# Kernel tuning notes

Hardware: AMD Instinct MI355X
Metric: run time of the kernel (lower is better)

Reference implementation:

```python
import jax, jax.numpy as jnp
import numpy as np

B, N_ATOMS = 8192, 64      # molecules, atoms per molecule
DIM, EXTRA, N_CLS = 70, 7, 11
N_FP = 10000               # fingerprint vocab


def setup_inputs() -> dict:
    key = jax.random.key(0)
    ks = jax.random.split(key, 9)
    atoms = jax.random.randint(ks[0], (B, N_ATOMS), 0, N_FP, dtype=jnp.int64 if jax.config.jax_enable_x64 else jnp.int32)
    adjacency = jax.random.uniform(ks[1], (B, N_ATOMS, N_ATOMS), dtype=jnp.float32)
    sel_desc = jax.random.normal(ks[2], (B, EXTRA), dtype=jnp.float32)
    embed_table = jax.random.normal(ks[3], (N_FP, DIM), dtype=jnp.float32)
    w1 = jax.random.normal(ks[4], (DIM, DIM), dtype=jnp.float32) * 0.05
    b1 = jax.random.normal(ks[5], (DIM,), dtype=jnp.float32) * 0.05
    w2 = jax.random.normal(ks[6], (DIM, DIM), dtype=jnp.float32) * 0.05
    b2 = jax.random.normal(ks[7], (DIM,), dtype=jnp.float32) * 0.05
    wp = jax.random.normal(ks[8], (DIM + EXTRA, N_CLS), dtype=jnp.float32) * 0.05
    bp = jnp.zeros((N_CLS,), dtype=jnp.float32)
    return {"atoms": atoms, "adjacency": adjacency, "sel_desc": sel_desc,
            "embed_table": embed_table, "w1": w1, "b1": b1,
            "w2": w2, "b2": b2, "wp": wp, "bp": bp}


def reference(atoms, adjacency, sel_desc, embed_table, w1, b1, w2, b2, wp, bp):
    # embed atoms: [B, n, dim]
    x = embed_table[atoms]
    # message-passing layers: relu(linear) then (block-diagonal == batched) adjacency matmul
    for w, b in ((w1, b1), (w2, b2)):
        h = jax.nn.relu(jnp.einsum('bnd,de->bne', x, w) + b)
        x = jnp.einsum('bnm,bmd->bnd', adjacency, h)
    # segment-sum pool over atoms per molecule (sum_axis)
    y = jnp.sum(x, axis=1)                       # [B, dim]
    y = jnp.concatenate([y, sel_desc], axis=1)   # [B, dim+extra]
    return jnp.einsum('bd,dc->bc', y, wp) + bp   # [B, 11]
```

## Files before the change

kernel.cpp:

```cpp
#include <hip/hip_runtime.h>
#include <hip/hip_bf16.h>

#define NFP    10000
#define DIM    70
#define GPAD   72
#define NATOMS 64
#define PGROWS 16

typedef short  short8  __attribute__((ext_vector_type(8)));
typedef float  floatx4 __attribute__((ext_vector_type(4)));

__device__ inline unsigned short f2bf(float f) {
  union { float f; unsigned u; } x; x.f = f;
  unsigned r = x.u + 0x7fffu + ((x.u >> 16) & 1u);
  return (unsigned short)(r >> 16);
}

__device__ inline ushort2 pk2bf(float a, float b) {
  __hip_bfloat162 h = __float22bfloat162_rn(make_float2(a, b));
  union { __hip_bfloat162 h; ushort2 u; } c; c.h = h; return c.u;
}

__global__ __launch_bounds__(256) void precompute_G(
    const float* __restrict__ emb, const float* __restrict__ w1,
    const float* __restrict__ b1,  const float* __restrict__ w2,
    unsigned short* __restrict__ G) {
  __shared__ float w1s[DIM * GPAD];
  __shared__ float w2s[DIM * GPAD];
  __shared__ float b1s[GPAD];
  __shared__ float embs[PGROWS * GPAD];
  __shared__ float e1s[PGROWS * GPAD];
  const int t = threadIdx.x;

  for (int i = t; i < DIM * GPAD; i += 256) {
    int r = i / GPAD, c = i % GPAD;
    float v1 = 0.f, v2 = 0.f;
    if (c < DIM) { v1 = w1[r * DIM + c]; v2 = w2[r * DIM + c]; }
    w1s[i] = v1; w2s[i] = v2;
  }
  if (t < GPAD) b1s[t] = (t < DIM) ? b1[t] : 0.f;
  const int row0 = blockIdx.x * PGROWS;
  for (int i = t; i < PGROWS * GPAD; i += 256) {
    int r = i / GPAD, c = i % GPAD;
    int vr = row0 + r;
    embs[i] = (vr < NFP && c < DIM) ? emb[vr * DIM + c] : 0.f;
  }
  __syncthreads();

  for (int task = t; task < PGROWS * 18; task += 256) {
    int r = task / 18, c4 = (task % 18) * 4;
    float4 acc = *(const float4*)&b1s[c4];
    for (int k = 0; k < DIM; k++) {
      float e = embs[r * GPAD + k];
      float4 w = *(const float4*)&w1s[k * GPAD + c4];
      acc.x = fmaf(e, w.x, acc.x); acc.y = fmaf(e, w.y, acc.y);
      acc.z = fmaf(e, w.z, acc.z); acc.w = fmaf(e, w.w, acc.w);
    }
    acc.x = fmaxf(acc.x, 0.f); acc.y = fmaxf(acc.y, 0.f);
    acc.z = fmaxf(acc.z, 0.f); acc.w = fmaxf(acc.w, 0.f);
    *(float4*)&e1s[r * GPAD + c4] = acc;
  }
  __syncthreads();

  for (int task = t; task < PGROWS * 18; task += 256) {
    int r = task / 18, c4 = (task % 18) * 4;
    int vr = row0 + r;
    if (vr >= NFP) continue;
    float ax = 0.f, ay = 0.f, az = 0.f, aw = 0.f;
    for (int k = 0; k < DIM; k++) {
      float e = e1s[r * GPAD + k];
      float4 w = *(const float4*)&w2s[k * GPAD + c4];
      ax = fmaf(e, w.x, ax); ay = fmaf(e, w.y, ay);
      az = fmaf(e, w.z, az); aw = fmaf(e, w.w, aw);
    }
    unsigned short* gp = G + vr * GPAD + c4;
    gp[0] = f2bf(ax); gp[1] = f2bf(ay); gp[2] = f2bf(az); gp[3] = f2bf(aw);
  }
}

__global__ __launch_bounds__(256, 6) void mol_fused(
    const int* __restrict__ atoms, const float* __restrict__ adj,
    const float* __restrict__ sel, const float* __restrict__ b2,
    const float* __restrict__ wp,  const float* __restrict__ bp,
    const unsigned short* __restrict__ G, float* __restrict__ out) {
  __shared__ unsigned short adjs[64 * GPAD];
  __shared__ unsigned short gTs[80 * GPAD];
  __shared__ float cwave[4 * 64];
  __shared__ float yacc[4 * 80];

  const int b = blockIdx.x;
  const int t = threadIdx.x;
  const int w = t >> 6, lane = t & 63;
  const int q = lane >> 4, li = lane & 15;
  const int R = w * 16;
  const int m = lane;

  const float* ap = adj + (size_t)b * 4096;
  const int mc = (t & 15) * 4;
  const int a  = t >> 4;
  float4 v0 = *(const float4*)(ap + (a     ) * 64 + mc);
  float4 v1 = *(const float4*)(ap + (a + 16) * 64 + mc);
  float4 v2 = *(const float4*)(ap + (a + 32) * 64 + mc);
  float4 v3 = *(const float4*)(ap + (a + 48) * 64 + mc);
  const int myAtom = atoms[b * 64 + m];
  const uint4* Gv = (const uint4*)G;
  uint4 g0 = Gv[(unsigned)myAtom * 9 + w];
  uint4 g1 = Gv[(unsigned)myAtom * 9 + w + 4];
  uint4 g2; g2.x = g2.y = g2.z = g2.w = 0u;
  if (w == 0) g2 = Gv[(unsigned)myAtom * 9 + 8];

  {
    float4 cs;
    cs.x = (v0.x + v1.x) + (v2.x + v3.x);
    cs.y = (v0.y + v1.y) + (v2.y + v3.y);
    cs.z = (v0.z + v1.z) + (v2.z + v3.z);
    cs.w = (v0.w + v1.w) + (v2.w + v3.w);
#pragma unroll
    for (int s = 16; s <= 32; s <<= 1) {
      cs.x += __shfl_xor(cs.x, s); cs.y += __shfl_xor(cs.y, s);
      cs.z += __shfl_xor(cs.z, s); cs.w += __shfl_xor(cs.w, s);
    }
    if (((t >> 4) & 3) == 0) *(float4*)&cwave[w * 64 + mc] = cs;

    float4 vv[4] = {v0, v1, v2, v3};
#pragma unroll
    for (int it = 0; it < 4; it++) {
      int n = a + 16 * it;
      ushort2 lo = pk2bf(vv[it].x, vv[it].y);
      ushort2 hi = pk2bf(vv[it].z, vv[it].w);
      ushort4 u; u.x = lo.x; u.y = lo.y; u.z = hi.x; u.w = hi.y;
      *(ushort4*)&adjs[n * GPAD + mc] = u;
    }
  }

  {
    unsigned short* gp0 = &gTs[(w * 8) * GPAD + m];
    gp0[0 * GPAD] = (unsigned short)(g0.x & 0xffff);
    gp0[1 * GPAD] = (unsigned short)(g0.x >> 16);
    gp0[2 * GPAD] = (unsigned short)(g0.y & 0xffff);
    gp0[3 * GPAD] = (unsigned short)(g0.y >> 16);
    gp0[4 * GPAD] = (unsigned short)(g0.z & 0xffff);
    gp0[5 * GPAD] = (unsigned short)(g0.z >> 16);
    gp0[6 * GPAD] = (unsigned short)(g0.w & 0xffff);
    gp0[7 * GPAD] = (unsigned short)(g0.w >> 16);
    unsigned short* gp1 = &gTs[((w + 4) * 8) * GPAD + m];
    gp1[0 * GPAD] = (unsigned short)(g1.x & 0xffff);
    gp1[1 * GPAD] = (unsigned short)(g1.x >> 16);
    gp1[2 * GPAD] = (unsigned short)(g1.y & 0xffff);
    gp1[3 * GPAD] = (unsigned short)(g1.y >> 16);
    gp1[4 * GPAD] = (unsigned short)(g1.z & 0xffff);
    gp1[5 * GPAD] = (unsigned short)(g1.z >> 16);
    gp1[6 * GPAD] = (unsigned short)(g1.w & 0xffff);
    gp1[7 * GPAD] = (unsigned short)(g1.w >> 16);
    if (w == 0) {
      unsigned short* gp2 = &gTs[64 * GPAD + m];
      gp2[0 * GPAD] = (unsigned short)(g2.x & 0xffff);
      gp2[1 * GPAD] = (unsigned short)(g2.x >> 16);
      gp2[2 * GPAD] = (unsigned short)(g2.y & 0xffff);
      gp2[3 * GPAD] = (unsigned short)(g2.y >> 16);
      gp2[4 * GPAD] = (unsigned short)(g2.z & 0xffff);
      gp2[5 * GPAD] = (unsigned short)(g2.z >> 16);
      gp2[6 * GPAD] = (unsigned short)(g2.w & 0xffff);
      gp2[7 * GPAD] = (unsigned short)(g2.w >> 16);
    }
  }
  __syncthreads();

  float cr[4];
  {
    float4 c0 = *(const float4*)&cwave[      R + q * 4];
    float4 c1 = *(const float4*)&cwave[ 64 + R + q * 4];
    float4 c2 = *(const float4*)&cwave[128 + R + q * 4];
    float4 c3 = *(const float4*)&cwave[192 + R + q * 4];
    cr[0] = (c0.x + c1.x) + (c2.x + c3.x);
    cr[1] = (c0.y + c1.y) + (c2.y + c3.y);
    cr[2] = (c0.z + c1.z) + (c2.z + c3.z);
    cr[3] = (c0.w + c1.w) + (c2.w + c3.w);
  }
  float bbv[5];
#pragma unroll
  for (int nt = 0; nt < 5; nt++) {
    int d = nt * 16 + li;
    bbv[nt] = (d < DIM) ? b2[d] : 0.f;
  }

  short8 a0 = *(const short8*)&adjs[(R + li) * GPAD + q * 8];
  short8 a1 = *(const short8*)&adjs[(R + li) * GPAD + 32 + q * 8];
  floatx4 acc[5];
#pragma unroll
  for (int nt = 0; nt < 5; nt++) {
    floatx4 z = {0.f, 0.f, 0.f, 0.f};
    short8 b0 = *(const short8*)&gTs[(nt * 16 + li) * GPAD + q * 8];
    short8 b1 = *(const short8*)&gTs[(nt * 16 + li) * GPAD + 32 + q * 8];
    z = __builtin_amdgcn_mfma_f32_16x16x32_bf16(a0, b0, z, 0, 0, 0);
    z = __builtin_amdgcn_mfma_f32_16x16x32_bf16(a1, b1, z, 0, 0, 0);
    acc[nt] = z;
  }

#pragma unroll
  for (int nt = 0; nt < 5; nt++) {
    float bb = bbv[nt];
    float p = 0.f;
#pragma unroll
    for (int r = 0; r < 4; r++)
      p = fmaf(cr[r], fmaxf(acc[nt][r] + bb, 0.f), p);
    p += __shfl_xor(p, 16);
    p += __shfl_xor(p, 32);
    if (q == 0) yacc[w * 80 + nt * 16 + li] = p;
  }
  __syncthreads();

  if (w == 0) {
    float* yv = cwave;
    yv[lane] = yacc[lane] + yacc[80 + lane] + yacc[160 + lane] + yacc[240 + lane];
    if (lane < 16) {
      int d2 = 64 + lane;
      float v2s = 0.f;
      if (lane < 6)
        v2s = yacc[d2] + yacc[80 + d2] + yacc[160 + d2] + yacc[240 + d2];
      else if (lane < 13)
        v2s = sel[(size_t)b * 7 + (d2 - DIM)];
      yv[d2] = v2s;
    }
    int c = lane & 15, qq = lane >> 4;
    float accp = 0.f;
    if (c < 11) {
#pragma unroll
      for (int j = 0; j < 20; j++) {
        int d = qq + 4 * j;
        int dd = (d < 77) ? d : 76;
        accp = fmaf(yv[d], wp[dd * 11 + c], accp);
      }
    }
    accp += __shfl_xor(accp, 16);
    accp += __shfl_xor(accp, 32);
    if (lane < 11) out[(size_t)b * 11 + lane] = accp + bp[lane];
  }
}

extern "C" void kernel_launch(void* const* d_in, const int* in_sizes, int n_in,
                              void* d_out, int out_size, void* d_ws, size_t ws_size,
                              hipStream_t stream) {
  const int*   atoms = (const int*)d_in[0];
  const float* adj   = (const float*)d_in[1];
  const float* sel   = (const float*)d_in[2];
  const float* emb   = (const float*)d_in[3];
  const float* w1    = (const float*)d_in[4];
  const float* b1    = (const float*)d_in[5];
  const float* w2    = (const float*)d_in[6];
  const float* b2    = (const float*)d_in[7];
  const float* wp    = (const float*)d_in[8];
  const float* bp    = (const float*)d_in[9];

  const int B = in_sizes[0] / NATOMS;
  unsigned short* G = (unsigned short*)d_ws;

  precompute_G<<<(NFP + PGROWS - 1) / PGROWS, 256, 0, stream>>>(emb, w1, b1, w2, G);
  mol_fused<<<B, 256, 0, stream>>>(atoms, adj, sel, b2, wp, bp, G, (float*)d_out);
}
```

Measured before the change: 233.1 us.

## Process four molecules per block with register prefetch of next molecule's data

```diff
diff --git a/kernel.cpp b/kernel.cpp
--- a/kernel.cpp
+++ b/kernel.cpp
@@ -6,6 +6,7 @@
 #define GPAD   72
 #define NATOMS 64
 #define PGROWS 16
+#define NMOL   4
 
 typedef short  short8  __attribute__((ext_vector_type(8)));
 typedef float  floatx4 __attribute__((ext_vector_type(4)));
@@ -78,7 +79,7 @@
   }
 }
 
-__global__ __launch_bounds__(256, 6) void mol_fused(
+__global__ __launch_bounds__(256, 4) void mol_fused(
     const int* __restrict__ atoms, const float* __restrict__ adj,
     const float* __restrict__ sel, const float* __restrict__ b2,
     const float* __restrict__ wp,  const float* __restrict__ bp,
@@ -87,154 +88,173 @@
   __shared__ unsigned short gTs[80 * GPAD];
   __shared__ float cwave[4 * 64];
   __shared__ float yacc[4 * 80];
-
-  const int b = blockIdx.x;
+  __shared__ float yv[80];
+
   const int t = threadIdx.x;
   const int w = t >> 6, lane = t & 63;
   const int q = lane >> 4, li = lane & 15;
   const int R = w * 16;
   const int m = lane;
-
-  const float* ap = adj + (size_t)b * 4096;
   const int mc = (t & 15) * 4;
   const int a  = t >> 4;
-  float4 v0 = *(const float4*)(ap + (a     ) * 64 + mc);
-  float4 v1 = *(const float4*)(ap + (a + 16) * 64 + mc);
-  float4 v2 = *(const float4*)(ap + (a + 32) * 64 + mc);
-  float4 v3 = *(const float4*)(ap + (a + 48) * 64 + mc);
-  const int myAtom = atoms[b * 64 + m];
+  const int mol0 = blockIdx.x * NMOL;
   const uint4* Gv = (const uint4*)G;
-  uint4 g0 = Gv[(unsigned)myAtom * 9 + w];
-  uint4 g1 = Gv[(unsigned)myAtom * 9 + w + 4];
-  uint4 g2; g2.x = g2.y = g2.z = g2.w = 0u;
-  if (w == 0) g2 = Gv[(unsigned)myAtom * 9 + 8];
-
-  {
-    float4 cs;
-    cs.x = (v0.x + v1.x) + (v2.x + v3.x);
-    cs.y = (v0.y + v1.y) + (v2.y + v3.y);
-    cs.z = (v0.z + v1.z) + (v2.z + v3.z);
-    cs.w = (v0.w + v1.w) + (v2.w + v3.w);
-#pragma unroll
-    for (int s = 16; s <= 32; s <<= 1) {
-      cs.x += __shfl_xor(cs.x, s); cs.y += __shfl_xor(cs.y, s);
-      cs.z += __shfl_xor(cs.z, s); cs.w += __shfl_xor(cs.w, s);
-    }
-    if (((t >> 4) & 3) == 0) *(float4*)&cwave[w * 64 + mc] = cs;
-
-    float4 vv[4] = {v0, v1, v2, v3};
-#pragma unroll
-    for (int it = 0; it < 4; it++) {
-      int n = a + 16 * it;
-      ushort2 lo = pk2bf(vv[it].x, vv[it].y);
-      ushort2 hi = pk2bf(vv[it].z, vv[it].w);
-      ushort4 u; u.x = lo.x; u.y = lo.y; u.z = hi.x; u.w = hi.y;
-      *(ushort4*)&adjs[n * GPAD + mc] = u;
-    }
-  }
-
-  {
-    unsigned short* gp0 = &gTs[(w * 8) * GPAD + m];
-    gp0[0 * GPAD] = (unsigned short)(g0.x & 0xffff);
-    gp0[1 * GPAD] = (unsigned short)(g0.x >> 16);
-    gp0[2 * GPAD] = (unsigned short)(g0.y & 0xffff);
-    gp0[3 * GPAD] = (unsigned short)(g0.y >> 16);
-    gp0[4 * GPAD] = (unsigned short)(g0.z & 0xffff);
-    gp0[5 * GPAD] = (unsigned short)(g0.z >> 16);
-    gp0[6 * GPAD] = (unsigned short)(g0.w & 0xffff);
-    gp0[7 * GPAD] = (unsigned short)(g0.w >> 16);
-    unsigned short* gp1 = &gTs[((w + 4) * 8) * GPAD + m];
-    gp1[0 * GPAD] = (unsigned short)(g1.x & 0xffff);
-    gp1[1 * GPAD] = (unsigned short)(g1.x >> 16);
-    gp1[2 * GPAD] = (unsigned short)(g1.y & 0xffff);
-    gp1[3 * GPAD] = (unsigned short)(g1.y >> 16);
-    gp1[4 * GPAD] = (unsigned short)(g1.z & 0xffff);
-    gp1[5 * GPAD] = (unsigned short)(g1.z >> 16);
-    gp1[6 * GPAD] = (unsigned short)(g1.w & 0xffff);
-    gp1[7 * GPAD] = (unsigned short)(g1.w >> 16);
+
+  int natom = atoms[mol0 * 64 + m];
+  const float* ap0 = adj + (size_t)mol0 * 4096;
+  float4 nv0 = *(const float4*)(ap0 + (a     ) * 64 + mc);
+  float4 nv1 = *(const float4*)(ap0 + (a + 16) * 64 + mc);
+  float4 nv2 = *(const float4*)(ap0 + (a + 32) * 64 + mc);
+  float4 nv3 = *(const float4*)(ap0 + (a + 48) * 64 + mc);
+  uint4 ng0 = Gv[(unsigned)natom * 9 + w];
+  uint4 ng1 = Gv[(unsigned)natom * 9 + w + 4];
+  uint4 ng2; ng2.x = ng2.y = ng2.z = ng2.w = 0u;
+  if (w == 0) ng2 = Gv[(unsigned)natom * 9 + 8];
+
+#pragma unroll
+  for (int i = 0; i < NMOL; i++) {
+    const int b = mol0 + i;
+
+    {
+      float4 cs;
+      cs.x = (nv0.x + nv1.x) + (nv2.x + nv3.x);
+      cs.y = (nv0.y + nv1.y) + (nv2.y + nv3.y);
+      cs.z = (nv0.z + nv1.z) + (nv2.z + nv3.z);
+      cs.w = (nv0.w + nv1.w) + (nv2.w + nv3.w);
+#pragma unroll
+      for (int s = 16; s <= 32; s <<= 1) {
+        cs.x += __shfl_xor(cs.x, s); cs.y += __shfl_xor(cs.y, s);
+        cs.z += __shfl_xor(cs.z, s); cs.w += __shfl_xor(cs.w, s);
+      }
+      if (((t >> 4) & 3) == 0) *(float4*)&cwave[w * 64 + mc] = cs;
+    }
+    {
+      float4 vv[4] = {nv0, nv1, nv2, nv3};
+#pragma unroll
+      for (int it = 0; it < 4; it++) {
+        int n = a + 16 * it;
+        ushort2 lo = pk2bf(vv[it].x, vv[it].y);
+        ushort2 hi = pk2bf(vv[it].z, vv[it].w);
+        ushort4 u; u.x = lo.x; u.y = lo.y; u.z = hi.x; u.w = hi.y;
+        *(ushort4*)&adjs[n * GPAD + mc] = u;
+      }
+    }
+    if (i + 1 < NMOL) {
+      natom = atoms[(b + 1) * 64 + m];
+      const float* apn = adj + (size_t)(b + 1) * 4096;
+      nv0 = *(const float4*)(apn + (a     ) * 64 + mc);
+      nv1 = *(const float4*)(apn + (a + 16) * 64 + mc);
+      nv2 = *(const float4*)(apn + (a + 32) * 64 + mc);
+      nv3 = *(const float4*)(apn + (a + 48) * 64 + mc);
+    }
+    {
+      unsigned short* gp0 = &gTs[(w * 8) * GPAD + m];
+      gp0[0 * GPAD] = (unsigned short)(ng0.x & 0xffff);
+      gp0[1 * GPAD] = (unsigned short)(ng0.x >> 16);
+      gp0[2 * GPAD] = (unsigned short)(ng0.y & 0xffff);
+      gp0[3 * GPAD] = (unsigned short)(ng0.y >> 16);
+      gp0[4 * GPAD] = (unsigned short)(ng0.z & 0xffff);
+      gp0[5 * GPAD] = (unsigned short)(ng0.z >> 16);
+      gp0[6 * GPAD] = (unsigned short)(ng0.w & 0xffff);
+      gp0[7 * GPAD] = (unsigned short)(ng0.w >> 16);
+      unsigned short* gp1 = &gTs[((w + 4) * 8) * GPAD + m];
+      gp1[0 * GPAD] = (unsigned short)(ng1.x & 0xffff);
+      gp1[1 * GPAD] = (unsigned short)(ng1.x >> 16);
+      gp1[2 * GPAD] = (unsigned short)(ng1.y & 0xffff);
+      gp1[3 * GPAD] = (unsigned short)(ng1.y >> 16);
+      gp1[4 * GPAD] = (unsigned short)(ng1.z & 0xffff);
+      gp1[5 * GPAD] = (unsigned short)(ng1.z >> 16);
+      gp1[6 * GPAD] = (unsigned short)(ng1.w & 0xffff);
+      gp1[7 * GPAD] = (unsigned short)(ng1.w >> 16);
+      if (w == 0) {
+        unsigned short* gp2 = &gTs[64 * GPAD + m];
+        gp2[0 * GPAD] = (unsigned short)(ng2.x & 0xffff);
+        gp2[1 * GPAD] = (unsigned short)(ng2.x >> 16);
+        gp2[2 * GPAD] = (unsigned short)(ng2.y & 0xffff);
+        gp2[3 * GPAD] = (unsigned short)(ng2.y >> 16);
+        gp2[4 * GPAD] = (unsigned short)(ng2.z & 0xffff);
+        gp2[5 * GPAD] = (unsigned short)(ng2.z >> 16);
+        gp2[6 * GPAD] = (unsigned short)(ng2.w & 0xffff);
+        gp2[7 * GPAD] = (unsigned short)(ng2.w >> 16);
+      }
+    }
+    if (i + 1 < NMOL) {
+      ng0 = Gv[(unsigned)natom * 9 + w];
+      ng1 = Gv[(unsigned)natom * 9 + w + 4];
+      ng2.x = ng2.y = ng2.z = ng2.w = 0u;
+      if (w == 0) ng2 = Gv[(unsigned)natom * 9 + 8];
+    }
+    __syncthreads();
+
+    float cr[4];
+    {
+      float4 c0 = *(const float4*)&cwave[      R + q * 4];
+      float4 c1 = *(const float4*)&cwave[ 64 + R + q * 4];
+      float4 c2 = *(const float4*)&cwave[128 + R + q * 4];
+      float4 c3 = *(const float4*)&cwave[192 + R + q * 4];
+      cr[0] = (c0.x + c1.x) + (c2.x + c3.x);
+      cr[1] = (c0.y + c1.y) + (c2.y + c3.y);
+      cr[2] = (c0.z + c1.z) + (c2.z + c3.z);
+      cr[3] = (c0.w + c1.w) + (c2.w + c3.w);
+    }
+    float bbv[5];
+#pragma unroll
+    for (int nt = 0; nt < 5; nt++) {
+      int d = nt * 16 + li;
+      bbv[nt] = (d < DIM) ? b2[d] : 0.f;
+    }
+
+    short8 a0 = *(const short8*)&adjs[(R + li) * GPAD + q * 8];
+    short8 a1 = *(const short8*)&adjs[(R + li) * GPAD + 32 + q * 8];
+    floatx4 acc[5];
+#pragma unroll
+    for (int nt = 0; nt < 5; nt++) {
+      floatx4 z = {0.f, 0.f, 0.f, 0.f};
+      short8 b0 = *(const short8*)&gTs[(nt * 16 + li) * GPAD + q * 8];
+      short8 b1 = *(const short8*)&gTs[(nt * 16 + li) * GPAD + 32 + q * 8];
+      z = __builtin_amdgcn_mfma_f32_16x16x32_bf16(a0, b0, z, 0, 0, 0);
+      z = __builtin_amdgcn_mfma_f32_16x16x32_bf16(a1, b1, z, 0, 0, 0);
+      acc[nt] = z;
+    }
+
+#pragma unroll
+    for (int nt = 0; nt < 5; nt++) {
+      float bb = bbv[nt];
+      float p = 0.f;
+#pragma unroll
+      for (int r = 0; r < 4; r++)
+        p = fmaf(cr[r], fmaxf(acc[nt][r] + bb, 0.f), p);
+      p += __shfl_xor(p, 16);
+      p += __shfl_xor(p, 32);
+      if (q == 0) yacc[w * 80 + nt * 16 + li] = p;
+    }
+    __syncthreads();
+
     if (w == 0) {
-      unsigned short* gp2 = &gTs[64 * GPAD + m];
-      gp2[0 * GPAD] = (unsigned short)(g2.x & 0xffff);
-      gp2[1 * GPAD] = (unsigned short)(g2.x >> 16);
-      gp2[2 * GPAD] = (unsigned short)(g2.y & 0xffff);
-      gp2[3 * GPAD] = (unsigned short)(g2.y >> 16);
-      gp2[4 * GPAD] = (unsigned short)(g2.z & 0xffff);
-      gp2[5 * GPAD] = (unsigned short)(g2.z >> 16);
-      gp2[6 * GPAD] = (unsigned short)(g2.w & 0xffff);
-      gp2[7 * GPAD] = (unsigned short)(g2.w >> 16);
-    }
-  }
-  __syncthreads();
-
-  float cr[4];
-  {
-    float4 c0 = *(const float4*)&cwave[      R + q * 4];
-    float4 c1 = *(const float4*)&cwave[ 64 + R + q * 4];
-    float4 c2 = *(const float4*)&cwave[128 + R + q * 4];
-    float4 c3 = *(const float4*)&cwave[192 + R + q * 4];
-    cr[0] = (c0.x + c1.x) + (c2.x + c3.x);
-    cr[1] = (c0.y + c1.y) + (c2.y + c3.y);
-    cr[2] = (c0.z + c1.z) + (c2.z + c3.z);
-    cr[3] = (c0.w + c1.w) + (c2.w + c3.w);
-  }
-  float bbv[5];
-#pragma unroll
-  for (int nt = 0; nt < 5; nt++) {
-    int d = nt * 16 + li;
-    bbv[nt] = (d < DIM) ? b2[d] : 0.f;
-  }
-
-  short8 a0 = *(const short8*)&adjs[(R + li) * GPAD + q * 8];
-  short8 a1 = *(const short8*)&adjs[(R + li) * GPAD + 32 + q * 8];
-  floatx4 acc[5];
-#pragma unroll
-  for (int nt = 0; nt < 5; nt++) {
-    floatx4 z = {0.f, 0.f, 0.f, 0.f};
-    short8 b0 = *(const short8*)&gTs[(nt * 16 + li) * GPAD + q * 8];
-    short8 b1 = *(const short8*)&gTs[(nt * 16 + li) * GPAD + 32 + q * 8];
-    z = __builtin_amdgcn_mfma_f32_16x16x32_bf16(a0, b0, z, 0, 0, 0);
-    z = __builtin_amdgcn_mfma_f32_16x16x32_bf16(a1, b1, z, 0, 0, 0);
-    acc[nt] = z;
-  }
-
-#pragma unroll
-  for (int nt = 0; nt < 5; nt++) {
-    float bb = bbv[nt];
-    float p = 0.f;
-#pragma unroll
-    for (int r = 0; r < 4; r++)
-      p = fmaf(cr[r], fmaxf(acc[nt][r] + bb, 0.f), p);
-    p += __shfl_xor(p, 16);
-    p += __shfl_xor(p, 32);
-    if (q == 0) yacc[w * 80 + nt * 16 + li] = p;
-  }
-  __syncthreads();
-
-  if (w == 0) {
-    float* yv = cwave;
-    yv[lane] = yacc[lane] + yacc[80 + lane] + yacc[160 + lane] + yacc[240 + lane];
-    if (lane < 16) {
-      int d2 = 64 + lane;
-      float v2s = 0.f;
-      if (lane < 6)
-        v2s = yacc[d2] + yacc[80 + d2] + yacc[160 + d2] + yacc[240 + d2];
-      else if (lane < 13)
-        v2s = sel[(size_t)b * 7 + (d2 - DIM)];
-      yv[d2] = v2s;
-    }
-    int c = lane & 15, qq = lane >> 4;
-    float accp = 0.f;
-    if (c < 11) {
-#pragma unroll
-      for (int j = 0; j < 20; j++) {
-        int d = qq + 4 * j;
-        int dd = (d < 77) ? d : 76;
-        accp = fmaf(yv[d], wp[dd * 11 + c], accp);
-      }
-    }
-    accp += __shfl_xor(accp, 16);
-    accp += __shfl_xor(accp, 32);
-    if (lane < 11) out[(size_t)b * 11 + lane] = accp + bp[lane];
+      yv[lane] = yacc[lane] + yacc[80 + lane] + yacc[160 + lane] + yacc[240 + lane];
+      if (lane < 16) {
+        int d2 = 64 + lane;
+        float v2s = 0.f;
+        if (lane < 6)
+          v2s = yacc[d2] + yacc[80 + d2] + yacc[160 + d2] + yacc[240 + d2];
+        else if (lane < 13)
+          v2s = sel[(size_t)b * 7 + (d2 - DIM)];
+        yv[d2] = v2s;
+      }
+      int c = lane & 15, qq = lane >> 4;
+      float accp = 0.f;
+      if (c < 11) {
+#pragma unroll
+        for (int j = 0; j < 20; j++) {
+          int d = qq + 4 * j;
+          int dd = (d < 77) ? d : 76;
+          accp = fmaf(yv[d], wp[dd * 11 + c], accp);
+        }
+      }
+      accp += __shfl_xor(accp, 16);
+      accp += __shfl_xor(accp, 32);
+      if (lane < 11) out[(size_t)b * 11 + lane] = accp + bp[lane];
+    }
   }
 }
 
@@ -256,5 +276,5 @@
   unsigned short* G = (unsigned short*)d_ws;
 
   precompute_G<<<(NFP + PGROWS - 1) / PGROWS, 256, 0, stream>>>(emb, w1, b1, w2, G);
-  mol_fused<<<B, 256, 0, stream>>>(atoms, adj, sel, b2, wp, bp, G, (float*)d_out);
-}
+  mol_fused<<<B / NMOL, 256, 0, stream>>>(atoms, adj, sel, b2, wp, bp, G, (float*)d_out);
+}
```

Measured after the change: 245.6 us. 5.4% more time.
